# Kernel optimization log

Hardware: AMD Instinct MI355X
Metric: run time of the kernel (lower is better)

## Reference

```python
import jax, jax.numpy as jnp
import numpy as np
import math

D = 512
H = 512

def setup_inputs() -> dict:
    key = jax.random.key(0)
    k1, k2, k3, k4 = jax.random.split(key, 4)
    x = jax.random.normal(k1, (64, 1024, D), dtype=jnp.float32)
    h0 = jax.random.normal(k2, (64, H), dtype=jnp.float32)
    Wx = jax.random.normal(k3, (D, 4 * H), dtype=jnp.float32) / math.sqrt(D)
    Wh = jax.random.normal(k4, (H, 4 * H), dtype=jnp.float32) / math.sqrt(H)
    b = jnp.zeros((4 * H,), dtype=jnp.float32)
    return {"x": x, "h0": h0, "Wx": Wx, "Wh": Wh, "b": b}

def reference(x, h0, Wx, Wh, b):
    # x: (N,T,D), h0: (N,H). Precompute input projections for all steps at once.
    Hd = h0.shape[-1]
    xW = jnp.einsum('ntd,df->ntf', x, Wx) + b  # (N,T,4H)

    def step(carry, xw_t):
        h, c = carry
        A = xw_t + h @ Wh  # (N,4H)
        i = jax.nn.sigmoid(A[:, :Hd])
        f = jax.nn.sigmoid(A[:, Hd:2 * Hd])
        o = jax.nn.sigmoid(A[:, 2 * Hd:3 * Hd])
        g = jnp.tanh(A[:, 3 * Hd:])
        c_next = f * c + i * g
        h_next = o * jnp.tanh(c_next)
        return (h_next, c_next), h_next

    c0 = jnp.zeros_like(h0)
    # scan over time axis: move T to leading dim
    _, hs = jax.lax.scan(step, (h0, c0), jnp.swapaxes(xW, 0, 1))  # (T,N,H)
    return jnp.swapaxes(hs, 0, 1)  # (N,T,H)
```

## Files before the change

kernel.cpp:

```cpp
#include <hip/hip_runtime.h>
#include <hip/hip_bf16.h>
#include <math.h>


#define TT 1024
#define HH 512
#define FH 2048
#define KK 1024
#define NN 64

typedef __attribute__((ext_vector_type(8))) short bf16x8;
typedef __attribute__((ext_vector_type(4))) float f32x4;
typedef __attribute__((ext_vector_type(4))) int int4v;
typedef __attribute__((ext_vector_type(2))) unsigned int uint2v;

__device__ __forceinline__ unsigned short f2bf(float f) {
    return __builtin_bit_cast(unsigned short, __float2bfloat16(f));
}

__global__ __launch_bounds__(256)
void prep_wt(const float* __restrict__ Wx, const float* __restrict__ Wh,
             unsigned short* __restrict__ Wt)
{
    __shared__ float tile[64][65];
    const int c0  = blockIdx.x * 64;
    const int k0  = blockIdx.y * 64;
    const int tid = threadIdx.x;

    #pragma unroll
    for (int it = 0; it < 16; ++it) {
        int idx = it * 256 + tid;
        int kk = idx >> 6, cc = idx & 63;
        int k = k0 + kk;
        float w = (k < 512) ? Wx[(size_t)k * FH + c0 + cc]
                            : Wh[(size_t)(k - 512) * FH + c0 + cc];
        tile[kk][cc] = w;
    }
    __syncthreads();

    #pragma unroll
    for (int it = 0; it < 8; ++it) {
        int idx = it * 256 + tid;
        int cc = idx >> 5, kp = idx & 31;
        unsigned int lo = f2bf(tile[kp * 2][cc]);
        unsigned int hi = f2bf(tile[kp * 2 + 1][cc]);
        *(unsigned int*)(Wt + (size_t)(c0 + cc) * KK + k0 + kp * 2) =
            lo | (hi << 16);
    }
}

__global__ __launch_bounds__(256)
void lstm_init(const float* __restrict__ h0, unsigned int* __restrict__ hb32)
{
    int id = blockIdx.x * 256 + threadIdx.x;
    if (id < NN * HH) {
        unsigned int v0 = (unsigned int)f2bf(h0[id]);
        unsigned int v1 = 0xFFFF0000u;
        unsigned int* p0 = hb32 + id;
        unsigned int* p1 = hb32 + NN * HH + id;
        asm volatile("global_store_dword %0, %1, off sc0 sc1" :: "v"(p0), "v"(v0) : "memory");
        asm volatile("global_store_dword %0, %1, off sc0 sc1" :: "v"(p1), "v"(v1) : "memory");
    }
}

__global__ __launch_bounds__(512)
void lstm_persist(const float* __restrict__ x,
                  const unsigned short* __restrict__ Wt,
                  const float* __restrict__ bias,
                  float* __restrict__ out,
                  unsigned int* __restrict__ hb32)
{
    __shared__ __align__(16) unsigned short Aph[16 * 512];
    __shared__ float part[8][16][17];

    const int tid  = threadIdx.x;
    const int wv   = tid >> 6;
    const int lane = tid & 63;
    const int l15  = lane & 15;
    const int kh   = lane >> 4;

    const int rg = blockIdx.x >> 6;
    const int jg = blockIdx.x & 63;
    const int j0 = jg * 8;
    const int rowbase = rg * 16;

    const int ct = wv & 1;
    const int kq = wv >> 1;

    const int lc   = ct * 16 + l15;
    const int gate = lc >> 3;
    const int jj   = lc & 7;
    const int gcol = gate * HH + j0 + jj;

    const unsigned short* wtp = Wt + (size_t)gcol * KK + kh * 8;
    bf16x8 bx[4], bh[4];
    #pragma unroll
    for (int ks = 0; ks < 4; ++ks) {
        bx[ks] = *(const bf16x8*)(wtp + kq * 128 + ks * 32);
        bh[ks] = *(const bf16x8*)(wtp + 512 + kq * 128 + ks * 32);
    }

    const float* xlane = x + (size_t)(rowbase + l15) * TT * 512 + kq * 128 + kh * 8;

    const int arow = l15;
    const int rsw  = ((arow & 15) << 3) | ((arow & 3) << 7);

    const int srow  = tid >> 5;
    const int scol  = tid & 31;
    const int rsw_s = ((srow & 15) << 3) | ((srow & 3) << 7);
    const unsigned int* hrow32 = hb32 + (size_t)(rowbase + srow) * HH + scol * 4;

    const int grow_l = (tid >> 3) & 15;
    const int q      = tid & 7;
    const int grow   = rowbase + grow_l;
    const int gj     = j0 + q;
    float bi = 0.f, bf_ = 0.f, bo = 0.f, bg = 0.f;
    if (tid < 128) {
        bi  = bias[gj];
        bf_ = bias[HH + gj];
        bo  = bias[2 * HH + gj];
        bg  = bias[3 * HH + gj];
    }
    float c_reg = 0.f;
    float* outp = out + (size_t)grow * TT * HH + gj;
    unsigned int* hdst32 = hb32 + (size_t)grow * HH + gj;

    int4v xw[8];
    {
        #pragma unroll
        for (int ks = 0; ks < 4; ++ks) {
            asm volatile("global_load_dwordx4 %0, %1, off" : "=v"(xw[2 * ks])     : "v"(xlane + ks * 32));
            asm volatile("global_load_dwordx4 %0, %1, off" : "=v"(xw[2 * ks + 1]) : "v"(xlane + ks * 32 + 4));
        }
        asm volatile("s_waitcnt vmcnt(0)" ::: "memory");
        __builtin_amdgcn_sched_barrier(0);
    }
    bf16x8 xf[4];
    #pragma unroll
    for (int ks = 0; ks < 4; ++ks) {
        float4 u = __builtin_bit_cast(float4, xw[2 * ks]);
        float4 v = __builtin_bit_cast(float4, xw[2 * ks + 1]);
        bf16x8 a;
        a[0] = (short)f2bf(u.x); a[1] = (short)f2bf(u.y);
        a[2] = (short)f2bf(u.z); a[3] = (short)f2bf(u.w);
        a[4] = (short)f2bf(v.x); a[5] = (short)f2bf(v.y);
        a[6] = (short)f2bf(v.z); a[7] = (short)f2bf(v.w);
        xf[ks] = a;
    }

    for (int t = 0; t < TT; ++t) {
        const int pb = t & 1;
        const unsigned int tg = (unsigned int)t;
        const unsigned int* hp = hrow32 + (size_t)pb * NN * HH;

        int4v hw[4];
        #pragma unroll
        for (int i = 0; i < 4; ++i) {
            asm volatile("global_load_dwordx4 %0, %1, off sc0 sc1"
                         : "=v"(hw[i]) : "v"(hp + i * 128));
        }

        f32x4 accx = {0.f, 0.f, 0.f, 0.f};
        #pragma unroll
        for (int ks = 0; ks < 4; ++ks)
            accx = __builtin_amdgcn_mfma_f32_16x16x32_bf16(xf[ks], bx[ks], accx, 0, 0, 0);

        asm volatile("s_waitcnt vmcnt(0)" ::: "memory");
        __builtin_amdgcn_sched_barrier(0);
        while (true) {
            int ok = 1;
            #pragma unroll
            for (int i = 0; i < 4; ++i) {
                #pragma unroll
                for (int e = 0; e < 4; ++e)
                    ok &= (int)((((unsigned int)hw[i][e]) >> 16) == tg);
            }
            if (__all(ok)) break;
            if (!ok) {
                #pragma unroll
                for (int i = 0; i < 4; ++i) {
                    asm volatile("global_load_dwordx4 %0, %1, off sc0 sc1"
                                 : "=v"(hw[i]) : "v"(hp + i * 128));
                }
            }
            asm volatile("s_waitcnt vmcnt(0)" ::: "memory");
            __builtin_amdgcn_sched_barrier(0);
        }

        #pragma unroll
        for (int i = 0; i < 4; ++i) {
            unsigned int lo = ((unsigned int)hw[i][0] & 0xFFFFu) | ((unsigned int)hw[i][1] << 16);
            unsigned int hi = ((unsigned int)hw[i][2] & 0xFFFFu) | ((unsigned int)hw[i][3] << 16);
            int s = (i * 128 + scol * 4) ^ rsw_s;
            uint2v pk = {lo, hi};
            *(uint2v*)(Aph + srow * 512 + s) = pk;
        }
        __syncthreads();

        f32x4 acch = {0.f, 0.f, 0.f, 0.f};
        #pragma unroll
        for (int ks = 0; ks < 4; ++ks) {
            bf16x8 hf = *(const bf16x8*)(Aph + arow * 512
                           + ((kq * 128 + ks * 32 + kh * 8) ^ rsw));
            acch = __builtin_amdgcn_mfma_f32_16x16x32_bf16(hf, bh[ks], acch, 0, 0, 0);
        }
        #pragma unroll
        for (int rr = 0; rr < 4; ++rr)
            part[wv][kh * 4 + rr][l15] = accx[rr] + acch[rr];
        __syncthreads();

        if (tid < 128) {
            float Ai = bi, Af = bf_, Ao = bo, Ag = bg;
            #pragma unroll
            for (int k2 = 0; k2 < 4; ++k2) {
                Ai += part[2 * k2][grow_l][q];
                Af += part[2 * k2][grow_l][8 + q];
                Ao += part[2 * k2 + 1][grow_l][q];
                Ag += part[2 * k2 + 1][grow_l][8 + q];
            }
            float ig = 1.f / (1.f + __expf(-Ai));
            float fg = 1.f / (1.f + __expf(-Af));
            float og = 1.f / (1.f + __expf(-Ao));
            float eg = __expf(2.f * Ag);
            float gg = 1.f - 2.f / (eg + 1.f);
            c_reg = fg * c_reg + ig * gg;
            float ec = __expf(2.f * c_reg);
            float tc = 1.f - 2.f / (ec + 1.f);
            float hn = og * tc;

            unsigned int hv = (((unsigned int)(t + 1)) << 16) | (unsigned int)f2bf(hn);
            unsigned int* hdst = hdst32 + (size_t)((t + 1) & 1) * NN * HH;
            asm volatile("global_store_dword %0, %1, off sc0 sc1"
                         :: "v"(hdst), "v"(hv) : "memory");
            outp[(size_t)t * HH] = hn;
        }

        if (t + 1 < TT) {
            const float* xp = xlane + (size_t)(t + 1) * 512;
            #pragma unroll
            for (int ks = 0; ks < 4; ++ks) {
                asm volatile("global_load_dwordx4 %0, %1, off" : "=v"(xw[2 * ks])     : "v"(xp + ks * 32));
                asm volatile("global_load_dwordx4 %0, %1, off" : "=v"(xw[2 * ks + 1]) : "v"(xp + ks * 32 + 4));
            }
            asm volatile("s_waitcnt vmcnt(0)" ::: "memory");
            __builtin_amdgcn_sched_barrier(0);
            #pragma unroll
            for (int ks = 0; ks < 4; ++ks) {
                float4 u = __builtin_bit_cast(float4, xw[2 * ks]);
                float4 v = __builtin_bit_cast(float4, xw[2 * ks + 1]);
                bf16x8 a;
                a[0] = (short)f2bf(u.x); a[1] = (short)f2bf(u.y);
                a[2] = (short)f2bf(u.z); a[3] = (short)f2bf(u.w);
                a[4] = (short)f2bf(v.x); a[5] = (short)f2bf(v.y);
                a[6] = (short)f2bf(v.z); a[7] = (short)f2bf(v.w);
                xf[ks] = a;
            }
        }
    }
}

extern "C" void kernel_launch(void* const* d_in, const int* in_sizes, int n_in,
                              void* d_out, int out_size, void* d_ws, size_t ws_size,
                              hipStream_t stream)
{
    const float* x  = (const float*)d_in[0];
    const float* h0 = (const float*)d_in[1];
    const float* Wx = (const float*)d_in[2];
    const float* Wh = (const float*)d_in[3];
    const float* b  = (const float*)d_in[4];
    float* out = (float*)d_out;

    char* ws = (char*)d_ws;
    unsigned short* Wt   = (unsigned short*)ws;
    unsigned int*   hb32 = (unsigned int*)(ws + (size_t)4 * 1024 * 1024);

    prep_wt<<<dim3(32, 16), 256, 0, stream>>>(Wx, Wh, Wt);
    lstm_init<<<128, 256, 0, stream>>>(h0, hb32);
    lstm_persist<<<256, 512, 0, stream>>>(x, Wt, b, out, hb32);
}
```

Baseline: 3.186 ms.

## Stage x tile cooperatively through LDS and prefetch next step asynchronously

Each thread now loads a contiguous 64-byte slice of the x rows for the block instead of each wave redundantly loading its own MFMA fragments. The slice is converted to bf16 and written into a swizzled LDS buffer that the MFMA reads from. The load for step t+1 is issued right after the h spin-wait, so it overlaps with the recurrent MFMA and gate math instead of stalling at the end of the step. The cost is an extra LDS buffer, an extra __syncthreads per step, and a vmcnt(0) at the top of each step that also waits on the outstanding out stores.

```diff
diff --git a/kernel.cpp b/kernel.cpp
--- a/kernel.cpp
+++ b/kernel.cpp
@@ -70,6 +70,7 @@
                   float* __restrict__ out,
                   unsigned int* __restrict__ hb32)
 {
+    __shared__ __align__(16) unsigned short Apx[16 * 512];
     __shared__ __align__(16) unsigned short Aph[16 * 512];
     __shared__ float part[8][16][17];
 
@@ -100,14 +101,13 @@
         bh[ks] = *(const bf16x8*)(wtp + 512 + kq * 128 + ks * 32);
     }
 
-    const float* xlane = x + (size_t)(rowbase + l15) * TT * 512 + kq * 128 + kh * 8;
-
     const int arow = l15;
     const int rsw  = ((arow & 15) << 3) | ((arow & 3) << 7);
 
     const int srow  = tid >> 5;
     const int scol  = tid & 31;
     const int rsw_s = ((srow & 15) << 3) | ((srow & 3) << 7);
+    const float* xrow = x + (size_t)(rowbase + srow) * TT * 512 + scol * 16;
     const unsigned int* hrow32 = hb32 + (size_t)(rowbase + srow) * HH + scol * 4;
 
     const int grow_l = (tid >> 3) & 15;
@@ -125,45 +125,44 @@
     float* outp = out + (size_t)grow * TT * HH + gj;
     unsigned int* hdst32 = hb32 + (size_t)grow * HH + gj;
 
-    int4v xw[8];
-    {
-        #pragma unroll
-        for (int ks = 0; ks < 4; ++ks) {
-            asm volatile("global_load_dwordx4 %0, %1, off" : "=v"(xw[2 * ks])     : "v"(xlane + ks * 32));
-            asm volatile("global_load_dwordx4 %0, %1, off" : "=v"(xw[2 * ks + 1]) : "v"(xlane + ks * 32 + 4));
-        }
-        asm volatile("s_waitcnt vmcnt(0)" ::: "memory");
-        __builtin_amdgcn_sched_barrier(0);
-    }
-    bf16x8 xf[4];
-    #pragma unroll
-    for (int ks = 0; ks < 4; ++ks) {
-        float4 u = __builtin_bit_cast(float4, xw[2 * ks]);
-        float4 v = __builtin_bit_cast(float4, xw[2 * ks + 1]);
-        bf16x8 a;
-        a[0] = (short)f2bf(u.x); a[1] = (short)f2bf(u.y);
-        a[2] = (short)f2bf(u.z); a[3] = (short)f2bf(u.w);
-        a[4] = (short)f2bf(v.x); a[5] = (short)f2bf(v.y);
-        a[6] = (short)f2bf(v.z); a[7] = (short)f2bf(v.w);
-        xf[ks] = a;
-    }
+    int4v xw[4];
+    #pragma unroll
+    for (int i = 0; i < 4; ++i)
+        asm volatile("global_load_dwordx4 %0, %1, off" : "=v"(xw[i]) : "v"(xrow + i * 4));
 
     for (int t = 0; t < TT; ++t) {
         const int pb = t & 1;
         const unsigned int tg = (unsigned int)t;
         const unsigned int* hp = hrow32 + (size_t)pb * NN * HH;
 
+        asm volatile("s_waitcnt vmcnt(0)" ::: "memory");
+        __builtin_amdgcn_sched_barrier(0);
+        {
+            unsigned int pk[8];
+            #pragma unroll
+            for (int i = 0; i < 4; ++i) {
+                float4 u = __builtin_bit_cast(float4, xw[i]);
+                pk[2 * i]     = (unsigned int)f2bf(u.x) | ((unsigned int)f2bf(u.y) << 16);
+                pk[2 * i + 1] = (unsigned int)f2bf(u.z) | ((unsigned int)f2bf(u.w) << 16);
+            }
+            *(int4v*)(Apx + srow * 512 + ((scol * 16) ^ rsw_s))       = *(int4v*)&pk[0];
+            *(int4v*)(Apx + srow * 512 + (((scol * 16) + 8) ^ rsw_s)) = *(int4v*)&pk[4];
+        }
         int4v hw[4];
         #pragma unroll
         for (int i = 0; i < 4; ++i) {
             asm volatile("global_load_dwordx4 %0, %1, off sc0 sc1"
                          : "=v"(hw[i]) : "v"(hp + i * 128));
         }
+        __syncthreads();
 
         f32x4 accx = {0.f, 0.f, 0.f, 0.f};
         #pragma unroll
-        for (int ks = 0; ks < 4; ++ks)
-            accx = __builtin_amdgcn_mfma_f32_16x16x32_bf16(xf[ks], bx[ks], accx, 0, 0, 0);
+        for (int ks = 0; ks < 4; ++ks) {
+            bf16x8 xf = *(const bf16x8*)(Apx + arow * 512
+                           + ((kq * 128 + ks * 32 + kh * 8) ^ rsw));
+            accx = __builtin_amdgcn_mfma_f32_16x16x32_bf16(xf, bx[ks], accx, 0, 0, 0);
+        }
 
         asm volatile("s_waitcnt vmcnt(0)" ::: "memory");
         __builtin_amdgcn_sched_barrier(0);
@@ -185,6 +184,13 @@
             }
             asm volatile("s_waitcnt vmcnt(0)" ::: "memory");
             __builtin_amdgcn_sched_barrier(0);
+        }
+
+        if (t + 1 < TT) {
+            const float* xp = xrow + (size_t)(t + 1) * 512;
+            #pragma unroll
+            for (int i = 0; i < 4; ++i)
+                asm volatile("global_load_dwordx4 %0, %1, off" : "=v"(xw[i]) : "v"(xp + i * 4));
         }
 
         #pragma unroll
@@ -234,28 +240,6 @@
                          :: "v"(hdst), "v"(hv) : "memory");
             outp[(size_t)t * HH] = hn;
         }
-
-        if (t + 1 < TT) {
-            const float* xp = xlane + (size_t)(t + 1) * 512;
-            #pragma unroll
-            for (int ks = 0; ks < 4; ++ks) {
-                asm volatile("global_load_dwordx4 %0, %1, off" : "=v"(xw[2 * ks])     : "v"(xp + ks * 32));
-                asm volatile("global_load_dwordx4 %0, %1, off" : "=v"(xw[2 * ks + 1]) : "v"(xp + ks * 32 + 4));
-            }
-            asm volatile("s_waitcnt vmcnt(0)" ::: "memory");
-            __builtin_amdgcn_sched_barrier(0);
-            #pragma unroll
-            for (int ks = 0; ks < 4; ++ks) {
-                float4 u = __builtin_bit_cast(float4, xw[2 * ks]);
-                float4 v = __builtin_bit_cast(float4, xw[2 * ks + 1]);
-                bf16x8 a;
-                a[0] = (short)f2bf(u.x); a[1] = (short)f2bf(u.y);
-                a[2] = (short)f2bf(u.z); a[3] = (short)f2bf(u.w);
-                a[4] = (short)f2bf(v.x); a[5] = (short)f2bf(v.y);
-                a[6] = (short)f2bf(v.z); a[7] = (short)f2bf(v.w);
-                xf[ks] = a;
-            }
-        }
     }
 }
 
```

After: 4.399 ms. 1.38x slower.
